# Kernel optimization log

Measured on AMD Instinct MI355X. Metric: run time of the kernel, lower is better.

## Reference

```python
import jax, jax.numpy as jnp
import numpy as np

B, N, D = 8, 2048, 256
K = 8
NP = 1024  # num_pooled = ceil(N * 0.5)
EPS = 1e-8
TEMP = 1.0


def setup_inputs() -> dict:
    key = jax.random.key(0)
    k1, k2, k3, k4 = jax.random.split(key, 4)
    tokens = jax.random.normal(k1, (B, N, D), dtype=jnp.float32)
    timestamps = jax.random.uniform(k2, (B, N), dtype=jnp.float32)
    W1 = jax.random.normal(k3, (2 * D, 128), dtype=jnp.float32) * 0.02
    b1 = jnp.zeros((128,), dtype=jnp.float32)
    W2 = jax.random.normal(k4, (128, NP), dtype=jnp.float32) * 0.02
    b2 = jnp.zeros((NP,), dtype=jnp.float32)
    return {"tokens": tokens, "timestamps": timestamps, "W1": W1, "b1": b1, "W2": W2, "b2": b2}


def _build_adjacency(tokens):
    # mutual-kNN graph on cosine similarity -> [B, N, N] float 0/1
    tn = tokens / (jnp.linalg.norm(tokens, axis=-1, keepdims=True) + EPS)
    sim = jnp.einsum("bnd,bmd->bnm", tn, tn)
    sim = jnp.where(jnp.eye(N, dtype=bool)[None], -jnp.inf, sim)  # no self (add_self=False)
    _, idx = jax.lax.top_k(sim, K)  # [B, N, K]
    bi = jnp.arange(B)[:, None, None]
    ri = jnp.arange(N)[None, :, None]
    adj = jnp.zeros((B, N, N), dtype=bool).at[bi, ri, idx].set(True)
    adj = adj & jnp.swapaxes(adj, 1, 2)  # mutual
    return adj.astype(jnp.float32)


def reference(tokens, timestamps, W1, b1, W2, b2):
    adjacency = _build_adjacency(tokens)

    # degree-normalized aggregation (use_gnn=True)
    degree = jnp.clip(adjacency.sum(axis=-1, keepdims=True), 1.0, None)
    agg = jnp.matmul(adjacency / degree, tokens)  # [B, N, D]
    features = jnp.concatenate([tokens, agg], axis=-1)  # [B, N, 2D]

    # assignment MLP (Linear -> exact GELU -> Linear), softmax over clusters
    h = jax.nn.gelu(features @ W1 + b1, approximate=False)
    logits = h @ W2 + b2  # [B, N, NP]
    assign = jax.nn.softmax(logits / TEMP, axis=-1)

    # soft-assignment pooling
    pooled_tokens = jnp.einsum("bnp,bnd->bpd", assign, tokens)  # [B, NP, D]
    pooled_t = jnp.einsum("bnp,bn->bp", assign, timestamps)  # [B, NP]

    # reorder pooled tokens by pooled timestamp
    sort_idx = jnp.argsort(pooled_t, axis=-1)
    pooled_tokens = jnp.take_along_axis(pooled_tokens, sort_idx[..., None], axis=1)
    pooled_t = jnp.take_along_axis(pooled_t, sort_idx, axis=1)

    # auxiliary losses
    assign_st = jnp.einsum("bnp,bmp->bnm", assign, assign)
    link_loss = jnp.mean((assign_st - adjacency) ** 2)
    entropy = jnp.mean(-jnp.sum(assign * jnp.log(assign + EPS), axis=-1))

    return pooled_tokens, pooled_t, link_loss, entropy
```

## Files before the change

kernel.cpp:

```cpp
#include <hip/hip_runtime.h>
#include <math.h>

#define B_ 8
#define N_ 2048
#define D_ 256
#define K_ 8
#define NP_ 1024
#define H_ 128
#define EPS_ 1e-8f
#define NEG_INF_ (-1e30f)

typedef unsigned int uint;
typedef unsigned short ushort;
typedef __attribute__((ext_vector_type(4))) float f32x4;
typedef __attribute__((ext_vector_type(8))) short short8;

__device__ __forceinline__ float gelu_exact(float x) {
    return 0.5f * x * (1.0f + erff(x * 0.70710678118654752440f));
}

__device__ __forceinline__ float dot4(float4 a, float4 b) {
    return a.x * b.x + a.y * b.y + a.z * b.z + a.w * b.w;
}

__device__ __forceinline__ ushort f2bf(float f) {
    uint u = __float_as_uint(f);
    u = (u + 0x7FFFu + ((u >> 16) & 1u)) >> 16;
    return (ushort)u;
}

__device__ __forceinline__ void gll16(const void* g, void* l) {
    __builtin_amdgcn_global_load_lds(
        (const __attribute__((address_space(1))) unsigned int*)g,
        (__attribute__((address_space(3))) unsigned int*)l, 16, 0, 0);
}

__device__ __forceinline__ float bsum256(float* red, int t, float v) {
    red[t] = v;
    __syncthreads();
#pragma unroll
    for (int s = 128; s > 0; s >>= 1) {
        if (t < s) red[t] += red[t + s];
        __syncthreads();
    }
    float r = red[0];
    __syncthreads();
    return r;
}

__device__ __forceinline__ float bmax256(float* red, int t, float v) {
    red[t] = v;
    __syncthreads();
#pragma unroll
    for (int s = 128; s > 0; s >>= 1) {
        if (t < s) red[t] = fmaxf(red[t], red[t + s]);
        __syncthreads();
    }
    float r = red[0];
    __syncthreads();
    return r;
}

__device__ __forceinline__ uint mono16(uint v) {
    return (v & 0x8000u) ? ((~v) & 0xFFFFu) : (v | 0x8000u);
}

__global__ __launch_bounds__(256) void k_norm(const float* __restrict__ tokens,
                                              float* __restrict__ tn,
                                              ushort* __restrict__ tnbf) {
    int row = blockIdx.x;
    int t = threadIdx.x;
    __shared__ float red[256];
    float x = tokens[(size_t)row * D_ + t];
    float ss = bsum256(red, t, x * x);
    float nrm = sqrtf(ss) + EPS_;
    float y = x / nrm;
    tn[(size_t)row * D_ + t] = y;
    tnbf[(size_t)row * D_ + t] = f2bf(y);
}

#define SCW_ 72
#define INSK_(L) { bool in_ = key > L; uint tm_ = L; L = in_ ? key : L; key = in_ ? tm_ : key; }
#define INS16_ INSK_(l0) INSK_(l1) INSK_(l2) INSK_(l3) INSK_(l4) INSK_(l5) INSK_(l6) INSK_(l7) \
               INSK_(l8) INSK_(l9) INSK_(l10) INSK_(l11) INSK_(l12) INSK_(l13) INSK_(l14) INSK_(l15)
#define INSM_ INSK_(m0) INSK_(m1) INSK_(m2) INSK_(m3) INSK_(m4) INSK_(m5) INSK_(m6) INSK_(m7) \
              INSK_(m8) INSK_(m9) INSK_(m10) INSK_(m11) INSK_(m12) INSK_(m13) INSK_(m14) INSK_(m15)

__global__ __launch_bounds__(256) void k_simtop(const ushort* __restrict__ tnbf,
                                                int* __restrict__ cands) {
    __shared__ __align__(16) char lds[53760];
    char* Bs = lds + 16384;
    ushort* sc = (ushort*)(lds + 49152);
    uint* mg = (uint*)(lds + 16384);

    int bid = blockIdx.x;
    int b = bid & 7;
    int panel = bid >> 3;
    int i0 = panel * 32;
    int t = threadIdx.x;
    int lane = t & 63;
    int wv = t >> 6;
    int rh = wv & 1, ch = wv >> 1;
    const char* tbb = (const char*)(tnbf + (size_t)b * N_ * D_);

#pragma unroll
    for (int c = 0; c < 4; ++c) {
        int e = (wv * 4 + c) * 64 + lane;
        int row = e >> 5, g = e & 31;
        gll16(tbb + (size_t)(i0 + row) * 512 + ((g ^ (row & 15)) << 4),
              lds + (wv * 4 + c) * 1024);
    }
    const char* gsrc[8];
#pragma unroll
    for (int c = 0; c < 8; ++c) {
        int e = (wv * 8 + c) * 64 + lane;
        int row = e >> 5, g = e & 31;
        gsrc[c] = tbb + (size_t)row * 512 + ((g ^ (row & 15)) << 4);
    }
#pragma unroll
    for (int c = 0; c < 8; ++c) {
        gll16(gsrc[c], Bs + (wv * 8 + c) * 1024);
        gsrc[c] += 32768;
    }
    asm volatile("s_waitcnt vmcnt(0)" ::: "memory");
    __syncthreads();

    int selrow = t >> 3;
    int selcs = t & 7;
    int gi = i0 + selrow;
    uint l0=0,l1=0,l2=0,l3=0,l4=0,l5=0,l6=0,l7=0,l8=0,l9=0,l10=0,l11=0,l12=0,l13=0,l14=0,l15=0;
    uint rth = 0;

    int arow = rh * 16 + (lane & 15);
    int brow0 = ch * 32 + (lane & 15);
    int brow1 = brow0 + 16;
    int scw = (rh * 16 + (lane >> 4) * 4) * SCW_ + ch * 32 + (lane & 15);

    for (int jt = 0; jt < 32; ++jt) {
        f32x4 acc0 = (f32x4){0.f, 0.f, 0.f, 0.f};
        f32x4 acc1 = (f32x4){0.f, 0.f, 0.f, 0.f};
#pragma unroll
        for (int ks = 0; ks < 8; ++ks) {
            int u = ks * 4 + (lane >> 4);
            short8 af = *(const short8*)(lds + arow * 512 + ((u ^ (arow & 15)) << 4));
            short8 bf0 = *(const short8*)(Bs + brow0 * 512 + ((u ^ (lane & 15)) << 4));
            short8 bf1 = *(const short8*)(Bs + brow1 * 512 + ((u ^ (lane & 15)) << 4));
            acc0 = __builtin_amdgcn_mfma_f32_16x16x32_bf16(af, bf0, acc0, 0, 0, 0);
            acc1 = __builtin_amdgcn_mfma_f32_16x16x32_bf16(af, bf1, acc1, 0, 0, 0);
        }
#pragma unroll
        for (int v = 0; v < 4; ++v) sc[scw + v * SCW_] = f2bf(acc0[v]);
#pragma unroll
        for (int v = 0; v < 4; ++v) sc[scw + v * SCW_ + 16] = f2bf(acc1[v]);
        __syncthreads();

        if (jt < 31) {
#pragma unroll
            for (int c = 0; c < 8; ++c) {
                gll16(gsrc[c], Bs + (wv * 8 + c) * 1024);
                gsrc[c] += 32768;
            }
        }
        int j0 = jt * 64;
        int sbase = selrow * SCW_;
        uint gate = l15 > rth ? l15 : rth;
#pragma unroll
        for (int jj = 0; jj < 8; ++jj) {
            int col = selcs + jj * 8;
            int j = j0 + col;
            uint sv = sc[sbase + col];
            if (j != gi) {
                uint key = (mono16(sv) << 16) | (65535u - (uint)j);
                if (key > gate) {
                    INS16_
                    gate = l15 > rth ? l15 : rth;
                }
            }
        }
        {
            uint m = l15;
            m = m > (uint)__shfl_xor((int)m, 1) ? m : (uint)__shfl_xor((int)m, 1);
            m = m > (uint)__shfl_xor((int)m, 2) ? m : (uint)__shfl_xor((int)m, 2);
            m = m > (uint)__shfl_xor((int)m, 4) ? m : (uint)__shfl_xor((int)m, 4);
            rth = m;
        }
        asm volatile("s_waitcnt vmcnt(0)" ::: "memory");
        __syncthreads();
    }

    uint* ml = mg + (size_t)t * 17;
    ml[0]=l0; ml[1]=l1; ml[2]=l2; ml[3]=l3; ml[4]=l4; ml[5]=l5; ml[6]=l6; ml[7]=l7;
    ml[8]=l8; ml[9]=l9; ml[10]=l10; ml[11]=l11; ml[12]=l12; ml[13]=l13; ml[14]=l14; ml[15]=l15;
    __syncthreads();
    if (selcs == 0) {
        uint m0=0,m1=0,m2=0,m3=0,m4=0,m5=0,m6=0,m7=0,m8=0,m9=0,m10=0,m11=0,m12=0,m13=0,m14=0,m15=0;
        const uint* base = mg + (size_t)(selrow * 8) * 17;
#pragma unroll
        for (int s2 = 0; s2 < 8; ++s2) {
            const uint* lp = base + s2 * 17;
            for (int q = 0; q < 16; ++q) {
                uint key = lp[q];
                if (key <= m15) break;
                INSM_
            }
        }
        int* crow = cands + ((size_t)b * N_ + gi) * 16;
        crow[0]=(int)(65535u-(m0&0xFFFFu));   crow[1]=(int)(65535u-(m1&0xFFFFu));
        crow[2]=(int)(65535u-(m2&0xFFFFu));   crow[3]=(int)(65535u-(m3&0xFFFFu));
        crow[4]=(int)(65535u-(m4&0xFFFFu));   crow[5]=(int)(65535u-(m5&0xFFFFu));
        crow[6]=(int)(65535u-(m6&0xFFFFu));   crow[7]=(int)(65535u-(m7&0xFFFFu));
        crow[8]=(int)(65535u-(m8&0xFFFFu));   crow[9]=(int)(65535u-(m9&0xFFFFu));
        crow[10]=(int)(65535u-(m10&0xFFFFu)); crow[11]=(int)(65535u-(m11&0xFFFFu));
        crow[12]=(int)(65535u-(m12&0xFFFFu)); crow[13]=(int)(65535u-(m13&0xFFFFu));
        crow[14]=(int)(65535u-(m14&0xFFFFu)); crow[15]=(int)(65535u-(m15&0xFFFFu));
    }
}

__global__ __launch_bounds__(64) void k_rescore(const float* __restrict__ tn,
                                                const int* __restrict__ cands,
                                                int* __restrict__ topk) {
    int row = blockIdx.x;
    int b = row >> 11;
    int lane = threadIdx.x;
    int j = cands[(size_t)row * 16 + (lane & 15)];
    float s = 0.f;
    if (lane < 16) {
        const float* ti = tn + (size_t)row * D_;
        const float* tj = tn + ((size_t)(b << 11) + j) * D_;
        for (int d = 0; d < D_; d += 4) {
            float4 u = *(const float4*)(tj + d);
            float4 w = *(const float4*)(ti + d);
            s += dot4(u, w);
        }
    }
    float dv[16];
    int jv[16];
#pragma unroll
    for (int c = 0; c < 16; ++c) {
        dv[c] = __shfl(s, c);
        jv[c] = __shfl(j, c);
    }
    uint used = 0;
    for (int r = 0; r < 8; ++r) {
        float bv = -1e38f;
        int bj = 1 << 30, bc = -1;
#pragma unroll
        for (int c = 0; c < 16; ++c) {
            bool av = !(used & (1u << c));
            bool better = av && (dv[c] > bv || (dv[c] == bv && jv[c] < bj));
            bv = better ? dv[c] : bv;
            bj = better ? jv[c] : bj;
            bc = better ? c : bc;
        }
        used |= 1u << bc;
        if (lane == 0) topk[(size_t)row * K_ + r] = bj;
    }
}

__global__ __launch_bounds__(64) void k_adj_agg(const float* __restrict__ tokens,
                                                const int* __restrict__ topk,
                                                int* __restrict__ nbr,
                                                int* __restrict__ deg,
                                                float* __restrict__ agg) {
    int row = blockIdx.x;
    int b = row >> 11;
    int i = row & (N_ - 1);
    int t = threadIdx.x;
    __shared__ int s_cand[K_];
    __shared__ int s_nbr[K_];
    __shared__ int s_deg;
    if (t < K_) {
        int j = topk[(size_t)row * K_ + t];
        const int* tj = topk + ((size_t)(b * N_ + j)) * K_;
        bool mut = false;
#pragma unroll
        for (int k = 0; k < K_; ++k) mut = mut || (tj[k] == i);
        s_cand[t] = mut ? j : -1;
    }
    __syncthreads();
    if (t == 0) {
        int d = 0;
#pragma unroll
        for (int k = 0; k < K_; ++k)
            if (s_cand[k] >= 0) s_nbr[d++] = s_cand[k];
        s_deg = d;
    }
    __syncthreads();
    int dgi = s_deg;
    const float* tb = tokens + (size_t)b * N_ * D_;
    float a0 = 0, a1 = 0, a2 = 0, a3 = 0;
    for (int k = 0; k < dgi; ++k) {
        float4 v = *(const float4*)(tb + (size_t)s_nbr[k] * D_ + t * 4);
        a0 += v.x; a1 += v.y; a2 += v.z; a3 += v.w;
    }
    float inv = 1.0f / (float)(dgi > 0 ? dgi : 1);
    *(float4*)(agg + (size_t)row * D_ + t * 4) = make_float4(a0 * inv, a1 * inv, a2 * inv, a3 * inv);
    if (t < K_) nbr[(size_t)row * K_ + t] = (t < dgi) ? s_nbr[t] : -1;
    if (t == 0) deg[row] = dgi;
}

__global__ __launch_bounds__(256) void k_tokT(const float* __restrict__ tokens,
                                              ushort* __restrict__ tokT) {
    int b = blockIdx.z;
    int n0 = blockIdx.x * 32, d0 = blockIdx.y * 32;
    __shared__ float tile[32][33];
    int t = threadIdx.x;
#pragma unroll
    for (int q = 0; q < 4; ++q) {
        int e = q * 256 + t;
        int r = e >> 5, c = e & 31;
        tile[r][c] = tokens[((size_t)b * N_ + n0 + r) * D_ + d0 + c];
    }
    __syncthreads();
#pragma unroll
    for (int q = 0; q < 4; ++q) {
        int e = q * 256 + t;
        int r = e >> 5, c = e & 31;
        tokT[((size_t)b * D_ + d0 + r) * N_ + n0 + c] = f2bf(tile[c][r]);
    }
}

__global__ __launch_bounds__(256) void k_asT(const float* __restrict__ assign,
                                             ushort* __restrict__ assignT) {
    int b = blockIdx.z;
    int n0 = blockIdx.x * 32, p0 = blockIdx.y * 32;
    __shared__ float tile[32][33];
    int t = threadIdx.x;
#pragma unroll
    for (int q = 0; q < 4; ++q) {
        int e = q * 256 + t;
        int r = e >> 5, c = e & 31;
        tile[r][c] = assign[((size_t)b * N_ + n0 + r) * NP_ + p0 + c];
    }
    __syncthreads();
#pragma unroll
    for (int q = 0; q < 4; ++q) {
        int e = q * 256 + t;
        int r = e >> 5, c = e & 31;
        assignT[((size_t)b * NP_ + p0 + r) * N_ + n0 + c] = f2bf(tile[c][r]);
    }
}

__global__ __launch_bounds__(256) void k_mlp12(const float* __restrict__ tokens,
                                               const float* __restrict__ agg,
                                               const float* __restrict__ W1,
                                               const float* __restrict__ b1,
                                               const float* __restrict__ W2,
                                               const float* __restrict__ b2,
                                               float* __restrict__ assign,
                                               float* __restrict__ ent_partial) {
    int row0 = blockIdx.x * 16;
    int t = threadIdx.x;
    int col = t & 127;
    int half = t >> 7;
    __shared__ __align__(16) char smem[32768];
    __shared__ float red[256];
    float* feat = (float*)smem;
    float* hsT = (float*)smem;
    float* red2 = (float*)(smem + 10240);

    for (int e = t; e < 16 * 2 * D_; e += 256) {
        int r = e >> 9, c = e & 511;
        feat[r * 512 + c] = (c < D_) ? tokens[(size_t)(row0 + r) * D_ + c]
                                     : agg[(size_t)(row0 + r) * D_ + (c - D_)];
    }
    __syncthreads();
    const float* fr = feat + (half * 8) * 512;
    float bias = b1[col];
    float a0 = bias, a1 = bias, a2 = bias, a3 = bias, a4 = bias, a5 = bias, a6 = bias, a7 = bias;
    for (int i = 0; i < 2 * D_; i += 4) {
        float w0 = W1[(size_t)(i + 0) * H_ + col];
        float w1 = W1[(size_t)(i + 1) * H_ + col];
        float w2 = W1[(size_t)(i + 2) * H_ + col];
        float w3 = W1[(size_t)(i + 3) * H_ + col];
        float4 f0 = *(const float4*)(fr + 0 * 512 + i);
        float4 f1 = *(const float4*)(fr + 1 * 512 + i);
        float4 f2 = *(const float4*)(fr + 2 * 512 + i);
        float4 f3 = *(const float4*)(fr + 3 * 512 + i);
        float4 f4 = *(const float4*)(fr + 4 * 512 + i);
        float4 f5 = *(const float4*)(fr + 5 * 512 + i);
        float4 f6 = *(const float4*)(fr + 6 * 512 + i);
        float4 f7 = *(const float4*)(fr + 7 * 512 + i);
        a0 += f0.x * w0; a0 += f0.y * w1; a0 += f0.z * w2; a0 += f0.w * w3;
        a1 += f1.x * w0; a1 += f1.y * w1; a1 += f1.z * w2; a1 += f1.w * w3;
        a2 += f2.x * w0; a2 += f2.y * w1; a2 += f2.z * w2; a2 += f2.w * w3;
        a3 += f3.x * w0; a3 += f3.y * w1; a3 += f3.z * w2; a3 += f3.w * w3;
        a4 += f4.x * w0; a4 += f4.y * w1; a4 += f4.z * w2; a4 += f4.w * w3;
        a5 += f5.x * w0; a5 += f5.y * w1; a5 += f5.z * w2; a5 += f5.w * w3;
        a6 += f6.x * w0; a6 += f6.y * w1; a6 += f6.z * w2; a6 += f6.w * w3;
        a7 += f7.x * w0; a7 += f7.y * w1; a7 += f7.z * w2; a7 += f7.w * w3;
    }
    float g0 = gelu_exact(a0), g1 = gelu_exact(a1), g2 = gelu_exact(a2), g3 = gelu_exact(a3);
    float g4 = gelu_exact(a4), g5 = gelu_exact(a5), g6 = gelu_exact(a6), g7 = gelu_exact(a7);
    __syncthreads();
    {
        int rb = half * 8;
        float* hp = hsT + col * 20 + rb;
        hp[0] = g0; hp[1] = g1; hp[2] = g2; hp[3] = g3;
        hp[4] = g4; hp[5] = g5; hp[6] = g6; hp[7] = g7;
    }
    __syncthreads();

    float acc[16][4];
#pragma unroll
    for (int s = 0; s < 4; ++s) {
        float bb = b2[s * 256 + t];
#pragma unroll
        for (int r = 0; r < 16; ++r) acc[r][s] = bb;
    }
#pragma unroll 4
    for (int i = 0; i < H_; ++i) {
        float w0 = W2[(size_t)i * NP_ + t];
        float w1 = W2[(size_t)i * NP_ + 256 + t];
        float w2 = W2[(size_t)i * NP_ + 512 + t];
        float w3 = W2[(size_t)i * NP_ + 768 + t];
        float hv[16];
        *(float4*)&hv[0] = *(const float4*)&hsT[i * 20 + 0];
        *(float4*)&hv[4] = *(const float4*)&hsT[i * 20 + 4];
        *(float4*)&hv[8] = *(const float4*)&hsT[i * 20 + 8];
        *(float4*)&hv[12] = *(const float4*)&hsT[i * 20 + 12];
#pragma unroll
        for (int r = 0; r < 16; ++r) {
            acc[r][0] += hv[r] * w0; acc[r][1] += hv[r] * w1;
            acc[r][2] += hv[r] * w2; acc[r][3] += hv[r] * w3;
        }
    }
#pragma unroll
    for (int r = 0; r < 16; ++r)
        red2[r * 256 + t] = fmaxf(fmaxf(acc[r][0], acc[r][1]), fmaxf(acc[r][2], acc[r][3]));
    __syncthreads();
#pragma unroll
    for (int s = 128; s > 0; s >>= 1) {
        if (t < s) {
#pragma unroll
            for (int r = 0; r < 16; ++r)
                red2[r * 256 + t] = fmaxf(red2[r * 256 + t], red2[r * 256 + t + s]);
        }
        __syncthreads();
    }
#pragma unroll
    for (int r = 0; r < 16; ++r) {
        float m = red2[r * 256];
        acc[r][0] -= m; acc[r][1] -= m; acc[r][2] -= m; acc[r][3] -= m;
    }
    __syncthreads();
#pragma unroll
    for (int r = 0; r < 16; ++r)
        red2[r * 256 + t] = expf(acc[r][0]) + expf(acc[r][1]) + expf(acc[r][2]) + expf(acc[r][3]);
    __syncthreads();
#pragma unroll
    for (int s = 128; s > 0; s >>= 1) {
        if (t < s) {
#pragma unroll
            for (int r = 0; r < 16; ++r) red2[r * 256 + t] += red2[r * 256 + t + s];
        }
        __syncthreads();
    }
    float entv = 0.f;
#pragma unroll
    for (int r = 0; r < 16; ++r) {
        float tot = red2[r * 256];
        float inv = 1.0f / tot;
        float p0 = expf(acc[r][0]) * inv, p1 = expf(acc[r][1]) * inv;
        float p2 = expf(acc[r][2]) * inv, p3 = expf(acc[r][3]) * inv;
        float* arow = assign + (size_t)(row0 + r) * NP_;
        arow[t] = p0; arow[256 + t] = p1; arow[512 + t] = p2; arow[768 + t] = p3;
        entv -= p0 * logf(p0 + EPS_) + p1 * logf(p1 + EPS_) + p2 * logf(p2 + EPS_) + p3 * logf(p3 + EPS_);
    }
    float bs = bsum256(red, t, entv);
    if (t == 0) ent_partial[blockIdx.x] = bs;
}

__device__ __forceinline__ void stage8k(const ushort* __restrict__ A,
                                        const ushort* __restrict__ B,
                                        int kb, char* lA, char* lB, int wv, int lane) {
#pragma unroll
    for (int c = 0; c < 2; ++c) {
        int e = (wv * 2 + c) * 64 + lane;
        int row = e >> 3, g = e & 7;
        size_t go = (size_t)row * N_ + kb + ((g ^ (row & 7)) << 3);
        gll16(A + go, lA + (wv * 2 + c) * 1024);
        gll16(B + go, lB + (wv * 2 + c) * 1024);
    }
}

__device__ __forceinline__ void gemm64g(const ushort* __restrict__ A,
                                        const ushort* __restrict__ B,
                                        f32x4 acc[2][2], char* lds) {
    int t = threadIdx.x;
    int lane = t & 63;
    int wv = t >> 6;
    int wm = wv >> 1, wn = wv & 1;
    stage8k(A, B, 0, lds, lds + 8192, wv, lane);
    for (int kb = 0; kb < N_; kb += 64) {
        int cur = (kb >> 6) & 1;
        char* lA = lds + cur * 16384;
        char* lB = lA + 8192;
        asm volatile("s_waitcnt vmcnt(0)" ::: "memory");
        __syncthreads();
        if (kb + 64 < N_) {
            char* nA = lds + (cur ^ 1) * 16384;
            stage8k(A, B, kb + 64, nA, nA + 8192, wv, lane);
        }
#pragma unroll
        for (int ks = 0; ks < 2; ++ks) {
            short8 afr[2], bfr[2];
#pragma unroll
            for (int f = 0; f < 2; ++f) {
                int rowA = wm * 32 + f * 16 + (lane & 15);
                int u = ks * 4 + (lane >> 4);
                afr[f] = *(const short8*)(lA + rowA * 128 + ((u ^ (rowA & 7)) << 4));
                int rowB = wn * 32 + f * 16 + (lane & 15);
                bfr[f] = *(const short8*)(lB + rowB * 128 + ((u ^ (rowB & 7)) << 4));
            }
#pragma unroll
            for (int fm = 0; fm < 2; ++fm)
#pragma unroll
                for (int fn = 0; fn < 2; ++fn)
                    acc[fm][fn] = __builtin_amdgcn_mfma_f32_16x16x32_bf16(
                        afr[fm], bfr[fn], acc[fm][fn], 0, 0, 0);
        }
    }
}

__global__ __launch_bounds__(256) void k_pool64(const ushort* __restrict__ assignT,
                                                const ushort* __restrict__ tokT,
                                                float* __restrict__ pooled) {
    __shared__ __align__(16) char lds[32768];
    int bid = blockIdx.x;
    int b = bid & 7;
    int tile = bid >> 3;
    int p0 = (tile >> 2) * 64, d0 = (tile & 3) * 64;
    const ushort* A = assignT + ((size_t)b * NP_ + p0) * N_;
    const ushort* Bp = tokT + ((size_t)b * D_ + d0) * N_;
    f32x4 acc[2][2];
#pragma unroll
    for (int x = 0; x < 2; ++x)
#pragma unroll
        for (int y = 0; y < 2; ++y) acc[x][y] = (f32x4){0.f, 0.f, 0.f, 0.f};
    gemm64g(A, Bp, acc, lds);
    int lane = threadIdx.x & 63;
    int wid = threadIdx.x >> 6;
    int wm = wid >> 1, wn = wid & 1;
#pragma unroll
    for (int fm = 0; fm < 2; ++fm)
#pragma unroll
        for (int fn = 0; fn < 2; ++fn) {
            int p = p0 + wm * 32 + fm * 16 + (lane >> 4) * 4;
            int d = d0 + wn * 32 + fn * 16 + (lane & 15);
#pragma unroll
            for (int v = 0; v < 4; ++v)
                pooled[((size_t)b * NP_ + p + v) * D_ + d] = acc[fm][fn][v];
        }
}

__global__ __launch_bounds__(256) void k_gram64(const ushort* __restrict__ assignT,
                                                float* __restrict__ gram_partial) {
    __shared__ __align__(16) char lds[32768];
    __shared__ float red[256];
    int bid = blockIdx.x;
    int b = bid & 7;
    int idx = bid >> 3;
    int ti = 0, rem = idx;
    while (rem >= 16 - ti) { rem -= 16 - ti; ++ti; }
    int tj = ti + rem;
    const ushort* A = assignT + ((size_t)b * NP_ + ti * 64) * N_;
    const ushort* Bp = assignT + ((size_t)b * NP_ + tj * 64) * N_;
    f32x4 acc[2][2];
#pragma unroll
    for (int x = 0; x < 2; ++x)
#pragma unroll
        for (int y = 0; y < 2; ++y) acc[x][y] = (f32x4){0.f, 0.f, 0.f, 0.f};
    gemm64g(A, Bp, acc, lds);
    float lsum = 0.f;
#pragma unroll
    for (int x = 0; x < 2; ++x)
#pragma unroll
        for (int y = 0; y < 2; ++y)
#pragma unroll
            for (int v = 0; v < 4; ++v) lsum += acc[x][y][v] * acc[x][y][v];
    float bs = bsum256(red, threadIdx.x, lsum);
    if (threadIdx.x == 0) gram_partial[(size_t)b * 136 + idx] = (ti == tj ? 1.0f : 2.0f) * bs;
}

__global__ __launch_bounds__(256) void k_poolt_part(const float* __restrict__ assign,
                                                    const float* __restrict__ ts,
                                                    float* __restrict__ part) {
    int bid = blockIdx.x;
    int b = bid & 7, ck = bid >> 3;
    int t = threadIdx.x;
    const float* A = assign + ((size_t)b * N_ + (size_t)ck * 64) * NP_;
    const float* T = ts + (size_t)b * N_ + (size_t)ck * 64;
    float4 acc = make_float4(0.f, 0.f, 0.f, 0.f);
    for (int n = 0; n < 64; ++n) {
        float4 v = *(const float4*)(A + (size_t)n * NP_ + t * 4);
        float tv = T[n];
        acc.x += v.x * tv; acc.y += v.y * tv; acc.z += v.z * tv; acc.w += v.w * tv;
    }
    *(float4*)(part + ((size_t)(b * 32 + ck)) * NP_ + t * 4) = acc;
}

__global__ __launch_bounds__(64) void k_edge(const float* __restrict__ assign,
                                             const int* __restrict__ nbr,
                                             const int* __restrict__ deg,
                                             float* __restrict__ edge_partial) {
    int row = blockIdx.x;
    int t = threadIdx.x;
    int dgi = deg[row];
    int b = row >> 11;
    float acc = 0.f;
    if (dgi > 0) {
        const float* ai = assign + (size_t)row * NP_;
        float areg[16];
#pragma unroll
        for (int q = 0; q < 16; ++q) areg[q] = ai[q * 64 + t];
        for (int k = 0; k < dgi; ++k) {
            int j = nbr[(size_t)row * K_ + k];
            const float* aj = assign + ((size_t)(b * N_ + j)) * NP_;
#pragma unroll
            for (int q = 0; q < 16; ++q) acc += areg[q] * aj[q * 64 + t];
        }
    }
#pragma unroll
    for (int s = 32; s > 0; s >>= 1) acc += __shfl_down(acc, s);
    if (t == 0) edge_partial[row] = acc;
}

__global__ __launch_bounds__(256) void k_sort(const float* __restrict__ part,
                                              float* __restrict__ out_pt,
                                              int* __restrict__ sortidx) {
    int b = blockIdx.x;
    int t = threadIdx.x;
    __shared__ float val[NP_];
    __shared__ int sidx[NP_];
    {
        float4 acc = make_float4(0.f, 0.f, 0.f, 0.f);
        for (int ck = 0; ck < 32; ++ck) {
            float4 v = *(const float4*)(part + ((size_t)(b * 32 + ck)) * NP_ + t * 4);
            acc.x += v.x; acc.y += v.y; acc.z += v.z; acc.w += v.w;
        }
        val[t * 4 + 0] = acc.x; val[t * 4 + 1] = acc.y;
        val[t * 4 + 2] = acc.z; val[t * 4 + 3] = acc.w;
        sidx[t * 4 + 0] = t * 4 + 0; sidx[t * 4 + 1] = t * 4 + 1;
        sidx[t * 4 + 2] = t * 4 + 2; sidx[t * 4 + 3] = t * 4 + 3;
    }
    __syncthreads();
    for (int k = 2; k <= NP_; k <<= 1) {
        for (int j = k >> 1; j > 0; j >>= 1) {
            for (int e = t; e < NP_; e += 256) {
                int l = e ^ j;
                if (l > e) {
                    bool up = ((e & k) == 0);
                    float v1 = val[e], v2 = val[l];
                    int i1 = sidx[e], i2 = sidx[l];
                    bool sw = up ? ((v1 > v2) || (v1 == v2 && i1 > i2))
                                 : ((v1 < v2) || (v1 == v2 && i1 < i2));
                    if (sw) { val[e] = v2; val[l] = v1; sidx[e] = i2; sidx[l] = i1; }
                }
            }
            __syncthreads();
        }
    }
    for (int e = t; e < NP_; e += 256) {
        out_pt[(size_t)b * NP_ + e] = val[e];
        sortidx[(size_t)b * NP_ + e] = sidx[e];
    }
}

__global__ __launch_bounds__(64) void k_gather(const float* __restrict__ pooledU,
                                               const int* __restrict__ sortidx,
                                               float* __restrict__ out) {
    int bp = blockIdx.x;
    int b = bp >> 10;
    int src = sortidx[bp];
    const float4* s = (const float4*)(pooledU + ((size_t)(b << 10) + src) * D_);
    float4* d = (float4*)(out + (size_t)bp * D_);
    d[threadIdx.x] = s[threadIdx.x];
}

__global__ __launch_bounds__(256) void k_fin(const float* __restrict__ gram_partial,
                                             const float* __restrict__ edge_partial,
                                             const float* __restrict__ ent_partial,
                                             const int* __restrict__ deg,
                                             float* __restrict__ out2) {
    int t = threadIdx.x;
    __shared__ float red[256];
    float t1 = 0.f, t2 = 0.f, t3 = 0.f, ent = 0.f;
    for (int i = t; i < 136 * B_; i += 256) t1 += gram_partial[i];
    for (int i = t; i < B_ * N_; i += 256) t2 += edge_partial[i];
    for (int i = t; i < (B_ * N_) / 16; i += 256) ent += ent_partial[i];
    for (int i = t; i < B_ * N_; i += 256) t3 += (float)deg[i];
    t1 = bsum256(red, t, t1);
    t2 = bsum256(red, t, t2);
    t3 = bsum256(red, t, t3);
    ent = bsum256(red, t, ent);
    if (t == 0) {
        out2[0] = (t1 - 2.f * t2 + t3) / (float)((size_t)B_ * N_ * N_);
        out2[1] = ent / (float)(B_ * N_);
    }
}

extern "C" void kernel_launch(void* const* d_in, const int* in_sizes, int n_in,
                              void* d_out, int out_size, void* d_ws, size_t ws_size,
                              hipStream_t stream) {
    const float* tokens = (const float*)d_in[0];
    const float* tstamp = (const float*)d_in[1];
    const float* W1 = (const float*)d_in[2];
    const float* b1 = (const float*)d_in[3];
    const float* W2 = (const float*)d_in[4];
    const float* b2 = (const float*)d_in[5];
    float* out = (float*)d_out;

    char* wsp = (char*)d_ws;
    size_t off = 0;
    auto alloc = [&](size_t bytes) -> void* {
        void* p = wsp + off;
        off += (bytes + 255) & ~(size_t)255;
        return p;
    };
    float* tn = (float*)alloc(sizeof(float) * (size_t)B_ * N_ * D_);
    float* agg = tn;
    float* assign = (float*)alloc(sizeof(float) * (size_t)B_ * N_ * NP_);
    ushort* tnbf = (ushort*)alloc(sizeof(ushort) * (size_t)B_ * N_ * D_);
    ushort* tokT = tnbf;
    ushort* assignT = (ushort*)alloc(sizeof(ushort) * (size_t)B_ * NP_ * N_);
    float* pooledU = (float*)alloc(sizeof(float) * (size_t)B_ * NP_ * D_);
    float* poolt_part = (float*)alloc(sizeof(float) * (size_t)B_ * 32 * NP_);
    int* candbuf = (int*)alloc(sizeof(int) * (size_t)B_ * N_ * 16);
    int* topkbuf = (int*)alloc(sizeof(int) * (size_t)B_ * N_ * K_);
    int* nbrbuf = (int*)alloc(sizeof(int) * (size_t)B_ * N_ * K_);
    int* degbuf = (int*)alloc(sizeof(int) * (size_t)B_ * N_);
    int* sortidx = (int*)alloc(sizeof(int) * (size_t)B_ * NP_);
    float* gram_p = (float*)alloc(sizeof(float) * 136 * B_);
    float* edge_p = (float*)alloc(sizeof(float) * (size_t)B_ * N_);
    float* ent_p = (float*)alloc(sizeof(float) * (size_t)(B_ * N_) / 16);

    k_norm<<<B_ * N_, 256, 0, stream>>>(tokens, tn, tnbf);
    k_simtop<<<512, 256, 0, stream>>>(tnbf, candbuf);
    k_rescore<<<B_ * N_, 64, 0, stream>>>(tn, candbuf, topkbuf);
    k_adj_agg<<<B_ * N_, 64, 0, stream>>>(tokens, topkbuf, nbrbuf, degbuf, agg);
    k_tokT<<<dim3(N_ / 32, D_ / 32, B_), 256, 0, stream>>>(tokens, tokT);
    k_mlp12<<<(B_ * N_) / 16, 256, 0, stream>>>(tokens, agg, W1, b1, W2, b2, assign, ent_p);
    k_asT<<<dim3(N_ / 32, NP_ / 32, B_), 256, 0, stream>>>(assign, assignT);
    k_pool64<<<512, 256, 0, stream>>>(assignT, tokT, pooledU);
    k_poolt_part<<<256, 256, 0, stream>>>(assign, tstamp, poolt_part);
    k_gram64<<<1088, 256, 0, stream>>>(assignT, gram_p);
    k_edge<<<B_ * N_, 64, 0, stream>>>(assign, nbrbuf, degbuf, edge_p);
    k_sort<<<B_, 256, 0, stream>>>(poolt_part, out + (size_t)B_ * NP_ * D_, sortidx);
    k_gather<<<B_ * NP_, 64, 0, stream>>>(pooledU, sortidx, out);
    k_fin<<<1, 256, 0, stream>>>(gram_p, edge_p, ent_p, degbuf,
                                 out + (size_t)B_ * NP_ * D_ + (size_t)B_ * NP_);
}
```

Before: 581.8 us.

## Merge independent kernels into block-indexed fused launches to cut launch count

```diff
diff --git a/kernel.cpp b/kernel.cpp
--- a/kernel.cpp
+++ b/kernel.cpp
@@ -41,19 +41,6 @@
 #pragma unroll
     for (int s = 128; s > 0; s >>= 1) {
         if (t < s) red[t] += red[t + s];
-        __syncthreads();
-    }
-    float r = red[0];
-    __syncthreads();
-    return r;
-}
-
-__device__ __forceinline__ float bmax256(float* red, int t, float v) {
-    red[t] = v;
-    __syncthreads();
-#pragma unroll
-    for (int s = 128; s > 0; s >>= 1) {
-        if (t < s) red[t] = fmaxf(red[t], red[t + s]);
         __syncthreads();
     }
     float r = red[0];
@@ -299,27 +286,6 @@
     if (t == 0) deg[row] = dgi;
 }
 
-__global__ __launch_bounds__(256) void k_tokT(const float* __restrict__ tokens,
-                                              ushort* __restrict__ tokT) {
-    int b = blockIdx.z;
-    int n0 = blockIdx.x * 32, d0 = blockIdx.y * 32;
-    __shared__ float tile[32][33];
-    int t = threadIdx.x;
-#pragma unroll
-    for (int q = 0; q < 4; ++q) {
-        int e = q * 256 + t;
-        int r = e >> 5, c = e & 31;
-        tile[r][c] = tokens[((size_t)b * N_ + n0 + r) * D_ + d0 + c];
-    }
-    __syncthreads();
-#pragma unroll
-    for (int q = 0; q < 4; ++q) {
-        int e = q * 256 + t;
-        int r = e >> 5, c = e & 31;
-        tokT[((size_t)b * D_ + d0 + r) * N_ + n0 + c] = f2bf(tile[c][r]);
-    }
-}
-
 __global__ __launch_bounds__(256) void k_asT(const float* __restrict__ assign,
                                              ushort* __restrict__ assignT) {
     int b = blockIdx.z;
@@ -341,20 +307,42 @@
     }
 }
 
-__global__ __launch_bounds__(256) void k_mlp12(const float* __restrict__ tokens,
-                                               const float* __restrict__ agg,
-                                               const float* __restrict__ W1,
-                                               const float* __restrict__ b1,
-                                               const float* __restrict__ W2,
-                                               const float* __restrict__ b2,
-                                               float* __restrict__ assign,
-                                               float* __restrict__ ent_partial) {
+__global__ __launch_bounds__(256) void k_m12t(const float* __restrict__ tokens,
+                                              const float* __restrict__ agg,
+                                              const float* __restrict__ W1,
+                                              const float* __restrict__ b1,
+                                              const float* __restrict__ W2,
+                                              const float* __restrict__ b2,
+                                              float* __restrict__ assign,
+                                              float* __restrict__ ent_partial,
+                                              ushort* __restrict__ tokT) {
+    __shared__ __align__(16) char smem[32768];
+    __shared__ float red[256];
+    int t = threadIdx.x;
+    if (blockIdx.x >= 1024) {
+        int sub = blockIdx.x - 1024;
+        int b = sub >> 9;
+        int d0 = ((sub >> 6) & 7) * 32;
+        int n0 = (sub & 63) * 32;
+        float* tile = (float*)smem;
+#pragma unroll
+        for (int q = 0; q < 4; ++q) {
+            int e = q * 256 + t;
+            int r = e >> 5, c = e & 31;
+            tile[r * 33 + c] = tokens[((size_t)b * N_ + n0 + r) * D_ + d0 + c];
+        }
+        __syncthreads();
+#pragma unroll
+        for (int q = 0; q < 4; ++q) {
+            int e = q * 256 + t;
+            int r = e >> 5, c = e & 31;
+            tokT[((size_t)b * D_ + d0 + r) * N_ + n0 + c] = f2bf(tile[c * 33 + r]);
+        }
+        return;
+    }
     int row0 = blockIdx.x * 16;
-    int t = threadIdx.x;
     int col = t & 127;
     int half = t >> 7;
-    __shared__ __align__(16) char smem[32768];
-    __shared__ float red[256];
     float* feat = (float*)smem;
     float* hsT = (float*)smem;
     float* red2 = (float*)(smem + 10240);
@@ -523,114 +511,132 @@
     }
 }
 
-__global__ __launch_bounds__(256) void k_pool64(const ushort* __restrict__ assignT,
-                                                const ushort* __restrict__ tokT,
-                                                float* __restrict__ pooled) {
-    __shared__ __align__(16) char lds[32768];
-    int bid = blockIdx.x;
-    int b = bid & 7;
-    int tile = bid >> 3;
-    int p0 = (tile >> 2) * 64, d0 = (tile & 3) * 64;
-    const ushort* A = assignT + ((size_t)b * NP_ + p0) * N_;
-    const ushort* Bp = tokT + ((size_t)b * D_ + d0) * N_;
-    f32x4 acc[2][2];
-#pragma unroll
-    for (int x = 0; x < 2; ++x)
-#pragma unroll
-        for (int y = 0; y < 2; ++y) acc[x][y] = (f32x4){0.f, 0.f, 0.f, 0.f};
-    gemm64g(A, Bp, acc, lds);
-    int lane = threadIdx.x & 63;
-    int wid = threadIdx.x >> 6;
-    int wm = wid >> 1, wn = wid & 1;
-#pragma unroll
-    for (int fm = 0; fm < 2; ++fm)
-#pragma unroll
-        for (int fn = 0; fn < 2; ++fn) {
-            int p = p0 + wm * 32 + fm * 16 + (lane >> 4) * 4;
-            int d = d0 + wn * 32 + fn * 16 + (lane & 15);
-#pragma unroll
-            for (int v = 0; v < 4; ++v)
-                pooled[((size_t)b * NP_ + p + v) * D_ + d] = acc[fm][fn][v];
-        }
-}
-
-__global__ __launch_bounds__(256) void k_gram64(const ushort* __restrict__ assignT,
-                                                float* __restrict__ gram_partial) {
+__global__ __launch_bounds__(256) void k_fuse4(const ushort* __restrict__ assignT,
+                                               const ushort* __restrict__ tokT,
+                                               const float* __restrict__ assign,
+                                               const float* __restrict__ tstamp,
+                                               const int* __restrict__ nbr,
+                                               const int* __restrict__ deg,
+                                               float* __restrict__ pooled,
+                                               float* __restrict__ part,
+                                               float* __restrict__ gram_partial,
+                                               float* __restrict__ edge_partial) {
     __shared__ __align__(16) char lds[32768];
     __shared__ float red[256];
     int bid = blockIdx.x;
-    int b = bid & 7;
-    int idx = bid >> 3;
-    int ti = 0, rem = idx;
-    while (rem >= 16 - ti) { rem -= 16 - ti; ++ti; }
-    int tj = ti + rem;
-    const ushort* A = assignT + ((size_t)b * NP_ + ti * 64) * N_;
-    const ushort* Bp = assignT + ((size_t)b * NP_ + tj * 64) * N_;
-    f32x4 acc[2][2];
-#pragma unroll
-    for (int x = 0; x < 2; ++x)
-#pragma unroll
-        for (int y = 0; y < 2; ++y) acc[x][y] = (f32x4){0.f, 0.f, 0.f, 0.f};
-    gemm64g(A, Bp, acc, lds);
-    float lsum = 0.f;
-#pragma unroll
-    for (int x = 0; x < 2; ++x)
-#pragma unroll
-        for (int y = 0; y < 2; ++y)
-#pragma unroll
-            for (int v = 0; v < 4; ++v) lsum += acc[x][y][v] * acc[x][y][v];
-    float bs = bsum256(red, threadIdx.x, lsum);
-    if (threadIdx.x == 0) gram_partial[(size_t)b * 136 + idx] = (ti == tj ? 1.0f : 2.0f) * bs;
-}
-
-__global__ __launch_bounds__(256) void k_poolt_part(const float* __restrict__ assign,
-                                                    const float* __restrict__ ts,
-                                                    float* __restrict__ part) {
-    int bid = blockIdx.x;
-    int b = bid & 7, ck = bid >> 3;
     int t = threadIdx.x;
-    const float* A = assign + ((size_t)b * N_ + (size_t)ck * 64) * NP_;
-    const float* T = ts + (size_t)b * N_ + (size_t)ck * 64;
-    float4 acc = make_float4(0.f, 0.f, 0.f, 0.f);
-    for (int n = 0; n < 64; ++n) {
-        float4 v = *(const float4*)(A + (size_t)n * NP_ + t * 4);
-        float tv = T[n];
-        acc.x += v.x * tv; acc.y += v.y * tv; acc.z += v.z * tv; acc.w += v.w * tv;
-    }
-    *(float4*)(part + ((size_t)(b * 32 + ck)) * NP_ + t * 4) = acc;
-}
-
-__global__ __launch_bounds__(64) void k_edge(const float* __restrict__ assign,
-                                             const int* __restrict__ nbr,
-                                             const int* __restrict__ deg,
-                                             float* __restrict__ edge_partial) {
-    int row = blockIdx.x;
+    if (bid < 1088) {
+        int b = bid & 7;
+        int idx = bid >> 3;
+        int ti = 0, rem = idx;
+        while (rem >= 16 - ti) { rem -= 16 - ti; ++ti; }
+        int tj = ti + rem;
+        const ushort* A = assignT + ((size_t)b * NP_ + ti * 64) * N_;
+        const ushort* Bp = assignT + ((size_t)b * NP_ + tj * 64) * N_;
+        f32x4 acc[2][2];
+#pragma unroll
+        for (int x = 0; x < 2; ++x)
+#pragma unroll
+            for (int y = 0; y < 2; ++y) acc[x][y] = (f32x4){0.f, 0.f, 0.f, 0.f};
+        gemm64g(A, Bp, acc, lds);
+        float lsum = 0.f;
+#pragma unroll
+        for (int x = 0; x < 2; ++x)
+#pragma unroll
+            for (int y = 0; y < 2; ++y)
+#pragma unroll
+                for (int v = 0; v < 4; ++v) lsum += acc[x][y][v] * acc[x][y][v];
+        float bs = bsum256(red, t, lsum);
+        if (t == 0) gram_partial[(size_t)b * 136 + idx] = (ti == tj ? 1.0f : 2.0f) * bs;
+    } else if (bid < 1600) {
+        int sub = bid - 1088;
+        int b = sub & 7;
+        int tile = sub >> 3;
+        int p0 = (tile >> 2) * 64, d0 = (tile & 3) * 64;
+        const ushort* A = assignT + ((size_t)b * NP_ + p0) * N_;
+        const ushort* Bp = tokT + ((size_t)b * D_ + d0) * N_;
+        f32x4 acc[2][2];
+#pragma unroll
+        for (int x = 0; x < 2; ++x)
+#pragma unroll
+            for (int y = 0; y < 2; ++y) acc[x][y] = (f32x4){0.f, 0.f, 0.f, 0.f};
+        gemm64g(A, Bp, acc, lds);
+        int lane = t & 63;
+        int wid = t >> 6;
+        int wm = wid >> 1, wn = wid & 1;
+#pragma unroll
+        for (int fm = 0; fm < 2; ++fm)
+#pragma unroll
+            for (int fn = 0; fn < 2; ++fn) {
+                int p = p0 + wm * 32 + fm * 16 + (lane >> 4) * 4;
+                int d = d0 + wn * 32 + fn * 16 + (lane & 15);
+#pragma unroll
+                for (int v = 0; v < 4; ++v)
+                    pooled[((size_t)b * NP_ + p + v) * D_ + d] = acc[fm][fn][v];
+            }
+    } else if (bid < 1856) {
+        int sub = bid - 1600;
+        int b = sub & 7, ck = sub >> 3;
+        const float* A = assign + ((size_t)b * N_ + (size_t)ck * 64) * NP_;
+        const float* T = tstamp + (size_t)b * N_ + (size_t)ck * 64;
+        float4 acc = make_float4(0.f, 0.f, 0.f, 0.f);
+        for (int n = 0; n < 64; ++n) {
+            float4 v = *(const float4*)(A + (size_t)n * NP_ + t * 4);
+            float tv = T[n];
+            acc.x += v.x * tv; acc.y += v.y * tv; acc.z += v.z * tv; acc.w += v.w * tv;
+        }
+        *(float4*)(part + ((size_t)(b * 32 + ck)) * NP_ + t * 4) = acc;
+    } else {
+        int row = (bid - 1856) * 4 + (t >> 6);
+        int lane = t & 63;
+        int dgi = deg[row];
+        int b = row >> 11;
+        float acc = 0.f;
+        if (dgi > 0) {
+            const float* ai = assign + (size_t)row * NP_;
+            float areg[16];
+#pragma unroll
+            for (int q = 0; q < 16; ++q) areg[q] = ai[q * 64 + lane];
+            for (int k = 0; k < dgi; ++k) {
+                int j = nbr[(size_t)row * K_ + k];
+                const float* aj = assign + ((size_t)(b * N_ + j)) * NP_;
+#pragma unroll
+                for (int q = 0; q < 16; ++q) acc += areg[q] * aj[q * 64 + lane];
+            }
+        }
+#pragma unroll
+        for (int s = 32; s > 0; s >>= 1) acc += __shfl_down(acc, s);
+        if (lane == 0) edge_partial[row] = acc;
+    }
+}
+
+__global__ __launch_bounds__(256) void k_sortfin(const float* __restrict__ part,
+                                                 float* __restrict__ out_pt,
+                                                 int* __restrict__ sortidx,
+                                                 const float* __restrict__ gram_partial,
+                                                 const float* __restrict__ edge_partial,
+                                                 const float* __restrict__ ent_partial,
+                                                 const int* __restrict__ deg,
+                                                 float* __restrict__ out2) {
     int t = threadIdx.x;
-    int dgi = deg[row];
-    int b = row >> 11;
-    float acc = 0.f;
-    if (dgi > 0) {
-        const float* ai = assign + (size_t)row * NP_;
-        float areg[16];
-#pragma unroll
-        for (int q = 0; q < 16; ++q) areg[q] = ai[q * 64 + t];
-        for (int k = 0; k < dgi; ++k) {
-            int j = nbr[(size_t)row * K_ + k];
-            const float* aj = assign + ((size_t)(b * N_ + j)) * NP_;
-#pragma unroll
-            for (int q = 0; q < 16; ++q) acc += areg[q] * aj[q * 64 + t];
-        }
-    }
-#pragma unroll
-    for (int s = 32; s > 0; s >>= 1) acc += __shfl_down(acc, s);
-    if (t == 0) edge_partial[row] = acc;
-}
-
-__global__ __launch_bounds__(256) void k_sort(const float* __restrict__ part,
-                                              float* __restrict__ out_pt,
-                                              int* __restrict__ sortidx) {
+    if (blockIdx.x == 8) {
+        __shared__ float red[256];
+        float t1 = 0.f, t2 = 0.f, t3 = 0.f, ent = 0.f;
+        for (int i = t; i < 136 * B_; i += 256) t1 += gram_partial[i];
+        for (int i = t; i < B_ * N_; i += 256) t2 += edge_partial[i];
+        for (int i = t; i < (B_ * N_) / 16; i += 256) ent += ent_partial[i];
+        for (int i = t; i < B_ * N_; i += 256) t3 += (float)deg[i];
+        t1 = bsum256(red, t, t1);
+        t2 = bsum256(red, t, t2);
+        t3 = bsum256(red, t, t3);
+        ent = bsum256(red, t, ent);
+        if (t == 0) {
+            out2[0] = (t1 - 2.f * t2 + t3) / (float)((size_t)B_ * N_ * N_);
+            out2[1] = ent / (float)(B_ * N_);
+        }
+        return;
+    }
     int b = blockIdx.x;
-    int t = threadIdx.x;
     __shared__ float val[NP_];
     __shared__ int sidx[NP_];
     {
@@ -676,28 +682,6 @@
     const float4* s = (const float4*)(pooledU + ((size_t)(b << 10) + src) * D_);
     float4* d = (float4*)(out + (size_t)bp * D_);
     d[threadIdx.x] = s[threadIdx.x];
-}
-
-__global__ __launch_bounds__(256) void k_fin(const float* __restrict__ gram_partial,
-                                             const float* __restrict__ edge_partial,
-                                             const float* __restrict__ ent_partial,
-                                             const int* __restrict__ deg,
-                                             float* __restrict__ out2) {
-    int t = threadIdx.x;
-    __shared__ float red[256];
-    float t1 = 0.f, t2 = 0.f, t3 = 0.f, ent = 0.f;
-    for (int i = t; i < 136 * B_; i += 256) t1 += gram_partial[i];
-    for (int i = t; i < B_ * N_; i += 256) t2 += edge_partial[i];
-    for (int i = t; i < (B_ * N_) / 16; i += 256) ent += ent_partial[i];
-    for (int i = t; i < B_ * N_; i += 256) t3 += (float)deg[i];
-    t1 = bsum256(red, t, t1);
-    t2 = bsum256(red, t, t2);
-    t3 = bsum256(red, t, t3);
-    ent = bsum256(red, t, ent);
-    if (t == 0) {
-        out2[0] = (t1 - 2.f * t2 + t3) / (float)((size_t)B_ * N_ * N_);
-        out2[1] = ent / (float)(B_ * N_);
-    }
 }
 
 extern "C" void kernel_launch(void* const* d_in, const int* in_sizes, int n_in,
@@ -739,15 +723,12 @@
     k_simtop<<<512, 256, 0, stream>>>(tnbf, candbuf);
     k_rescore<<<B_ * N_, 64, 0, stream>>>(tn, candbuf, topkbuf);
     k_adj_agg<<<B_ * N_, 64, 0, stream>>>(tokens, topkbuf, nbrbuf, degbuf, agg);
-    k_tokT<<<dim3(N_ / 32, D_ / 32, B_), 256, 0, stream>>>(tokens, tokT);
-    k_mlp12<<<(B_ * N_) / 16, 256, 0, stream>>>(tokens, agg, W1, b1, W2, b2, assign, ent_p);
+    k_m12t<<<5120, 256, 0, stream>>>(tokens, agg, W1, b1, W2, b2, assign, ent_p, tokT);
     k_asT<<<dim3(N_ / 32, NP_ / 32, B_), 256, 0, stream>>>(assign, assignT);
-    k_pool64<<<512, 256, 0, stream>>>(assignT, tokT, pooledU);
-    k_poolt_part<<<256, 256, 0, stream>>>(assign, tstamp, poolt_part);
-    k_gram64<<<1088, 256, 0, stream>>>(assignT, gram_p);
-    k_edge<<<B_ * N_, 64, 0, stream>>>(assign, nbrbuf, degbuf, edge_p);
-    k_sort<<<B_, 256, 0, stream>>>(poolt_part, out + (size_t)B_ * NP_ * D_, sortidx);
+    k_fuse4<<<5952, 256, 0, stream>>>(assignT, tokT, assign, tstamp, nbrbuf, degbuf,
+                                      pooledU, poolt_part, gram_p, edge_p);
+    k_sortfin<<<9, 256, 0, stream>>>(poolt_part, out + (size_t)B_ * NP_ * D_, sortidx,
+                                     gram_p, edge_p, ent_p, degbuf,
+                                     out + (size_t)B_ * NP_ * D_ + (size_t)B_ * NP_);
     k_gather<<<B_ * NP_, 64, 0, stream>>>(pooledU, sortidx, out);
-    k_fin<<<1, 256, 0, stream>>>(gram_p, edge_p, ent_p, degbuf,
-                                 out + (size_t)B_ * NP_ * D_ + (size_t)B_ * NP_);
-}
+}
```

Measured after the change: 507.1 us (median of 2 runs). 12.9% less time.
